# Kernel tuning notes

Hardware: AMD Instinct MI355X
Metric: run time of the kernel (lower is better)

## Reference

```python
import jax, jax.numpy as jnp
import numpy as np

N, E, NFEAT, NHID, K, TOP_N, NCLASS = 50000, 800000, 512, 128, 4, 2, 64
ALPHA = 0.2   # LeakyReLU negative slope (config.alpha)
EPS = 1e-16   # avoid 0/0 for isolated / fully-masked nodes


def _spgat_layer(h, src, dst, a, mask, concat):
    """SpGraphAttentionLayer_2: attention over given edges, no internal W.
    h: (N, F); a: (2F,); mask: optional (E,) 0/1 edge-subset mask.
    edge_e = exp(-leakyrelu(a . [h_src; h_dst]));
    out = segsum(e * h_dst) / segsum(e)  (per target node src).
    """
    F = h.shape[1]
    s1 = h @ a[:F]                     # (N,)
    s2 = h @ a[F:]                     # (N,)
    e = jnp.exp(-jax.nn.leaky_relu(s1[src] + s2[dst], ALPHA))  # (E,)
    if mask is not None:
        e = e * mask
    rowsum = jax.ops.segment_sum(e, src, num_segments=N)              # (N,)
    hp = jax.ops.segment_sum(e[:, None] * h[dst], src, num_segments=N)  # (N,F)
    hp = hp / (rowsum[:, None] + EPS)
    return jax.nn.elu(hp) if concat else hp


def setup_inputs() -> dict:
    key = jax.random.key(0)
    ks = jax.random.split(key, 7)
    x = jax.random.normal(ks[0], (N, NFEAT), jnp.float32)
    edge = jax.random.randint(ks[1], (2, E), 0, N)
    W_ks = jax.random.normal(ks[2], (K, NFEAT, NHID), jnp.float32) * 0.05
    a_k = jax.random.normal(ks[3], (K, 2 * NHID * K), jnp.float32) * 0.05
    W_o = jax.random.normal(ks[4], (NHID * K, NCLASS), jnp.float32) * 0.05
    a_att = jax.random.normal(ks[5], (K, 2 * NHID), jnp.float32) * 0.05
    a_out = jax.random.normal(ks[6], (2 * NCLASS,), jnp.float32) * 0.05
    return {"x": x, "edge": edge, "W_ks": W_ks, "a_k": a_k,
            "W_o": W_o, "a_att": a_att, "a_out": a_out}


def reference(x, edge, W_ks, a_k, W_o, a_att, a_out):
    src, dst = edge[0], edge[1]
    # K per-factor projections; dropout is a no-op in eval mode
    h_k = jnp.einsum('nf,kfh->knh', x, W_ks)              # (K, N, H)
    h = jnp.transpose(h_k, (1, 0, 2)).reshape(N, K * NHID)  # cat(h_k, dim=1)
    # Edge-level factor routing: softmax_K( a_k @ [h_src; h_dst] ).
    # Linear score => precompute per-node halves instead of (E, 2KH) gather.
    s_src = h @ a_k[:, :K * NHID].T                       # (N, K)
    s_dst = h @ a_k[:, K * NHID:].T                       # (N, K)
    edge_att = jax.nn.softmax(s_src[src] + s_dst[dst], axis=-1)  # (E, K)
    top_att, top_idx = jax.lax.top_k(edge_att, TOP_N)     # (E, TOP_N)
    # edge e belongs to factor k iff k is among its top_n factors
    masks = (top_idx[:, :, None] == jnp.arange(K)[None, None, :]).any(1)  # (E, K)
    outs = [_spgat_layer(h_k[k], src, dst, a_att[k],
                         masks[:, k].astype(h.dtype), True) for k in range(K)]
    xo = jnp.concatenate(outs, axis=1) @ W_o              # (N, NCLASS)
    xo = jax.nn.elu(_spgat_layer(xo, src, dst, a_out, None, False))
    att_loss = jnp.mean(1.0 - jnp.sum(top_att, axis=1))
    return jax.nn.log_softmax(xo, axis=1), att_loss
```

## Files before the change

kernel.cpp:

```cpp
#include <hip/hip_runtime.h>
#include <math.h>

#define NN 50000
#define NE 800000
#define NF 512
#define NH 128
#define KF 4
#define NC 64
#define LRELU_ALPHA 0.2f
#define EPSF 1e-16f

typedef unsigned short u16;
typedef __attribute__((ext_vector_type(8))) short bf16x8;
typedef __attribute__((ext_vector_type(4))) float f32x4;

#define OFF_H      0LL
#define OFF_HP     (OFF_H + (long long)NN * NF)
#define OFF_REC    (OFF_HP + (long long)NN * NF)
#define OFF_XO0    (OFF_REC + 4LL * NE)
#define OFF_SSRC   (OFF_XO0 + (long long)NN * NC)
#define OFF_SDST   (OFF_SSRC + (long long)NN * KF)
#define OFF_S1A    (OFF_SDST + (long long)NN * KF)
#define OFF_S2A    (OFF_S1A + (long long)NN * KF)
#define OFF_ROWSUM (OFF_S2A + (long long)NN * KF)
#define OFF_S1O    (OFF_ROWSUM + (long long)NN * KF)
#define OFF_S2O    (OFF_S1O + NN)
#define OFF_START  (OFF_S2O + NN)
#define OFF_CNT    (OFF_START + NN + 4)
#define OFF_CURSOR (OFF_CNT + NN)
#define OFF_ATT    (OFF_CURSOR + NN)
#define WS_FLOATS  (OFF_ATT + 2)

__device__ __forceinline__ u16 bf16_rne(float f) {
    unsigned int u = __float_as_uint(f);
    return (u16)((u + 0x7FFFu + ((u >> 16) & 1u)) >> 16);
}
__device__ __forceinline__ float bf16_f(u16 b) {
    return __uint_as_float(((unsigned int)b) << 16);
}

__device__ __forceinline__ void gload_lds16(const u16* g, u16* l) {
    __builtin_amdgcn_global_load_lds(
        (const __attribute__((address_space(1))) void*)g,
        (__attribute__((address_space(3))) void*)l, 16, 0, 0);
}

__global__ __launch_bounds__(256) void split_x(const float* __restrict__ x,
                                               u16* __restrict__ xhi,
                                               u16* __restrict__ xlo) {
    size_t i = ((size_t)blockIdx.x * 256 + threadIdx.x) * 8;
    float4 v0 = *(const float4*)(x + i);
    float4 v1 = *(const float4*)(x + i + 4);
    float v[8] = {v0.x, v0.y, v0.z, v0.w, v1.x, v1.y, v1.z, v1.w};
    unsigned int hp[4], lp[4];
#pragma unroll
    for (int j = 0; j < 4; ++j) {
        u16 h0 = bf16_rne(v[2 * j]);
        u16 h1 = bf16_rne(v[2 * j + 1]);
        u16 l0 = bf16_rne(v[2 * j] - bf16_f(h0));
        u16 l1 = bf16_rne(v[2 * j + 1] - bf16_f(h1));
        hp[j] = (unsigned int)h0 | ((unsigned int)h1 << 16);
        lp[j] = (unsigned int)l0 | ((unsigned int)l1 << 16);
    }
    *(uint4*)(xhi + i) = make_uint4(hp[0], hp[1], hp[2], hp[3]);
    *(uint4*)(xlo + i) = make_uint4(lp[0], lp[1], lp[2], lp[3]);
}

__global__ void split_w(const float* __restrict__ Wks,
                        u16* __restrict__ wthi, u16* __restrict__ wtlo) {
    int b = blockIdx.x;
    int kf = b >> 7, n = b & 127;
    for (int f = threadIdx.x; f < NF; f += 256) {
        float v = Wks[(size_t)kf * (NF * NH) + (size_t)f * NH + n];
        u16 hb = bf16_rne(v);
        u16 lb = bf16_rne(v - bf16_f(hb));
        wthi[(size_t)b * NF + f] = hb;
        wtlo[(size_t)b * NF + f] = lb;
    }
}

__global__ __launch_bounds__(256) void gemm_h_mfma(
        const u16* __restrict__ xhi, const u16* __restrict__ xlo,
        const u16* __restrict__ wthi, const u16* __restrict__ wtlo,
        float* __restrict__ h) {
    __shared__ u16 Ah[128 * 32], Al[128 * 32], Bh[128 * 32], Bl[128 * 32];
    int m0 = blockIdx.y * 128, n0 = blockIdx.x * 128;
    int tid = threadIdx.x;
    int lane = tid & 63;
    int wave = tid >> 6, wm = wave >> 1, wn = wave & 1;
    f32x4 acc[4][4];
#pragma unroll
    for (int i = 0; i < 4; ++i)
#pragma unroll
        for (int j = 0; j < 4; ++j) acc[i][j] = (f32x4)(0.f);

    u16* sbuf = (wave == 0) ? Ah : (wave == 1) ? Al : (wave == 2) ? Bh : Bl;
    const u16* gbase = (wave == 0) ? xhi : (wave == 1) ? xlo
                     : (wave == 2) ? wthi : wtlo;
    int rowbase = (wave < 2) ? m0 : n0;
    int c16s = (lane & 3) ^ ((lane >> 2) & 3) ^ (lane >> 4);
    const u16* gsrc[8];
#pragma unroll
    for (int i = 0; i < 8; ++i) {
        int rowg = rowbase + 16 * i + (lane >> 2);
        if (wave < 2 && rowg >= NN) rowg = NN - 1;
        gsrc[i] = gbase + (size_t)rowg * NF + c16s * 8;
    }

    const int arow = wm * 64 + (lane & 15);
    const int brow = wn * 64 + (lane & 15);
    const int rc16 = (lane >> 4) ^ ((lane & 3) ^ ((lane >> 2) & 3));
    const int fragoff = rc16 * 8;

    for (int k0 = 0; k0 < NF; k0 += 32) {
        __syncthreads();
#pragma unroll
        for (int i = 0; i < 8; ++i)
            gload_lds16(gsrc[i] + k0, sbuf + i * 512);
        __syncthreads();
        bf16x8 ah[4], al[4], bh[4], bl[4];
#pragma unroll
        for (int mi = 0; mi < 4; ++mi) {
            ah[mi] = *(const bf16x8*)(Ah + (arow + mi * 16) * 32 + fragoff);
            al[mi] = *(const bf16x8*)(Al + (arow + mi * 16) * 32 + fragoff);
        }
#pragma unroll
        for (int ni = 0; ni < 4; ++ni) {
            bh[ni] = *(const bf16x8*)(Bh + (brow + ni * 16) * 32 + fragoff);
            bl[ni] = *(const bf16x8*)(Bl + (brow + ni * 16) * 32 + fragoff);
        }
#pragma unroll
        for (int mi = 0; mi < 4; ++mi)
#pragma unroll
            for (int ni = 0; ni < 4; ++ni) {
                acc[mi][ni] = __builtin_amdgcn_mfma_f32_16x16x32_bf16(
                    ah[mi], bh[ni], acc[mi][ni], 0, 0, 0);
                acc[mi][ni] = __builtin_amdgcn_mfma_f32_16x16x32_bf16(
                    ah[mi], bl[ni], acc[mi][ni], 0, 0, 0);
                acc[mi][ni] = __builtin_amdgcn_mfma_f32_16x16x32_bf16(
                    al[mi], bh[ni], acc[mi][ni], 0, 0, 0);
            }
    }
#pragma unroll
    for (int mi = 0; mi < 4; ++mi) {
        int mbase = m0 + wm * 64 + mi * 16 + (lane >> 4) * 4;
#pragma unroll
        for (int ni = 0; ni < 4; ++ni) {
            int n = n0 + wn * 64 + ni * 16 + (lane & 15);
#pragma unroll
            for (int r = 0; r < 4; ++r) {
                int m = mbase + r;
                if (m < NN) h[(size_t)m * NF + n] = acc[mi][ni][r];
            }
        }
    }
}

__global__ __launch_bounds__(256) void compute_svals_h(
        const float* __restrict__ h, const float* __restrict__ a_k,
        const float* __restrict__ a_att,
        float* __restrict__ s_src, float* __restrict__ s_dst,
        float* __restrict__ s1a, float* __restrict__ s2a) {
    __shared__ float Ak[4][1024];
    __shared__ float Aa[4][256];
    for (int i = threadIdx.x; i < 4096; i += 256) Ak[i >> 10][i & 1023] = a_k[i];
    for (int i = threadIdx.x; i < 1024; i += 256) Aa[i >> 8][i & 255] = a_att[i];
    __syncthreads();
    int w = threadIdx.x >> 6, lane = threadIdx.x & 63;
    for (int n = blockIdx.x * 4 + w; n < NN; n += gridDim.x * 4) {
        const float* hr = h + (size_t)n * NF;
        float accS[4] = {0, 0, 0, 0}, accD[4] = {0, 0, 0, 0};
        float accQ1[4] = {0, 0, 0, 0}, accQ2[4] = {0, 0, 0, 0};
#pragma unroll
        for (int i = 0; i < 8; ++i) {
            int f = i * 64 + lane;
            float hv = hr[f];
#pragma unroll
            for (int k = 0; k < 4; ++k) {
                accS[k] = fmaf(hv, Ak[k][f], accS[k]);
                accD[k] = fmaf(hv, Ak[k][512 + f], accD[k]);
            }
            accQ1[i >> 1] = fmaf(hv, Aa[i >> 1][f & 127], accQ1[i >> 1]);
            accQ2[i >> 1] = fmaf(hv, Aa[i >> 1][128 + (f & 127)], accQ2[i >> 1]);
        }
#pragma unroll
        for (int off = 32; off >= 1; off >>= 1) {
#pragma unroll
            for (int k = 0; k < 4; ++k) {
                accS[k] += __shfl_xor(accS[k], off);
                accD[k] += __shfl_xor(accD[k], off);
                accQ1[k] += __shfl_xor(accQ1[k], off);
                accQ2[k] += __shfl_xor(accQ2[k], off);
            }
        }
        if (lane == 0) {
#pragma unroll
            for (int k = 0; k < 4; ++k) {
                s_src[n * 4 + k] = accS[k];
                s_dst[n * 4 + k] = accD[k];
                s1a[n * 4 + k]   = accQ1[k];
                s2a[n * 4 + k]   = accQ2[k];
            }
        }
    }
}

__global__ void csr_count(const int* __restrict__ edge, int* __restrict__ cnt) {
    int e = blockIdx.x * 256 + threadIdx.x;
    if (e < NE) atomicAdd(&cnt[edge[e]], 1);
}

__global__ __launch_bounds__(1024) void csr_scan(const int* __restrict__ cnt,
                                                 int* __restrict__ start) {
    __shared__ int part[1024];
    int t = threadIdx.x;
    const int CH = (NN + 1023) / 1024;
    int base = t * CH;
    int s = 0;
    for (int i = 0; i < CH; ++i) {
        int idx = base + i;
        if (idx < NN) s += cnt[idx];
    }
    part[t] = s;
    __syncthreads();
    for (int off = 1; off < 1024; off <<= 1) {
        int v = (t >= off) ? part[t - off] : 0;
        __syncthreads();
        part[t] += v;
        __syncthreads();
    }
    int run = (t == 0) ? 0 : part[t - 1];
    for (int i = 0; i < CH; ++i) {
        int idx = base + i;
        if (idx < NN) { start[idx] = run; run += cnt[idx]; }
    }
    if (t == 1023) start[NN] = run;
}

__global__ __launch_bounds__(256) void edge_pre1(
        const int* __restrict__ edge, const int* __restrict__ start,
        int* __restrict__ cursor,
        const float* __restrict__ s_src, const float* __restrict__ s_dst,
        const float* __restrict__ s1a, const float* __restrict__ s2a,
        int4* __restrict__ rec, double* __restrict__ att_acc) {
    __shared__ float blk[4];
    int tid = threadIdx.x;
    int e = blockIdx.x * 256 + tid;
    float t2 = 0.f;
    if (e < NE) {
        int src = edge[e];
        int dst = edge[NE + e];
        float4 ss = *(const float4*)(s_src + (size_t)src * 4);
        float4 sd = *(const float4*)(s_dst + (size_t)dst * 4);
        float l0 = ss.x + sd.x, l1 = ss.y + sd.y, l2 = ss.z + sd.z, l3 = ss.w + sd.w;
        int i1 = 0; float v1 = l0;
        if (l1 > v1) { v1 = l1; i1 = 1; }
        if (l2 > v1) { v1 = l2; i1 = 2; }
        if (l3 > v1) { v1 = l3; i1 = 3; }
        int i2 = 0; float v2 = -3.4e38f;
        if (i1 != 0)            { v2 = l0; i2 = 0; }
        if (i1 != 1 && l1 > v2) { v2 = l1; i2 = 1; }
        if (i1 != 2 && l2 > v2) { v2 = l2; i2 = 2; }
        if (i1 != 3 && l3 > v2) { v2 = l3; i2 = 3; }
        float esum = expf(l0 - v1) + expf(l1 - v1) + expf(l2 - v1) + expf(l3 - v1);
        t2 = (1.f + expf(v2 - v1)) / esum;
        float4 q1 = *(const float4*)(s1a + (size_t)src * 4);
        float4 q2 = *(const float4*)(s2a + (size_t)dst * 4);
        float q1v1 = i1 == 0 ? q1.x : i1 == 1 ? q1.y : i1 == 2 ? q1.z : q1.w;
        float q2v1 = i1 == 0 ? q2.x : i1 == 1 ? q2.y : i1 == 2 ? q2.z : q2.w;
        float q1v2 = i2 == 0 ? q1.x : i2 == 1 ? q1.y : i2 == 2 ? q1.z : q1.w;
        float q2v2 = i2 == 0 ? q2.x : i2 == 1 ? q2.y : i2 == 2 ? q2.z : q2.w;
        float sv1 = q1v1 + q2v1, sv2 = q1v2 + q2v2;
        float ee1 = expf(-(sv1 >= 0.f ? sv1 : LRELU_ALPHA * sv1));
        float ee2 = expf(-(sv2 >= 0.f ? sv2 : LRELU_ALPHA * sv2));
        int p = start[src] + atomicAdd(&cursor[src], 1);
        rec[p] = make_int4(dst, src | (i1 << 16) | (i2 << 18),
                           __float_as_int(ee1), __float_as_int(ee2));
    }
#pragma unroll
    for (int off = 32; off >= 1; off >>= 1) t2 += __shfl_xor(t2, off);
    if ((tid & 63) == 0) blk[tid >> 6] = t2;
    __syncthreads();
    if (tid == 0)
        atomicAdd(att_acc, (double)(blk[0] + blk[1] + blk[2] + blk[3]));
}

__global__ __launch_bounds__(256) void node_gather1(
        const int* __restrict__ start, const int4* __restrict__ rec,
        const float* __restrict__ h, float* __restrict__ hp,
        float* __restrict__ rowsum) {
    __shared__ float red[4][512];
    __shared__ float rsred[4][4];
    int n = blockIdx.x;
    int w = threadIdx.x >> 6, lane = threadIdx.x & 63;
    int j0 = start[n], j1 = start[n + 1];
    float a00 = 0.f, a01 = 0.f, a10 = 0.f, a11 = 0.f;
    float a20 = 0.f, a21 = 0.f, a30 = 0.f, a31 = 0.f;
    float rs0 = 0.f, rs1 = 0.f, rs2 = 0.f, rs3 = 0.f;
    for (int j = j0 + w; j < j1; j += 4) {
        int4 r = rec[j];
        int i1 = (r.y >> 16) & 3, i2 = (r.y >> 18) & 3;
        float w1 = __int_as_float(r.z), w2 = __int_as_float(r.w);
        const float* hr = h + (size_t)r.x * NF + lane;
        float v1a = hr[i1 * 128];
        float v1b = hr[i1 * 128 + 64];
        float v2a = hr[i2 * 128];
        float v2b = hr[i2 * 128 + 64];
        switch (i1) {
            case 0: a00 = fmaf(w1, v1a, a00); a01 = fmaf(w1, v1b, a01); rs0 += w1; break;
            case 1: a10 = fmaf(w1, v1a, a10); a11 = fmaf(w1, v1b, a11); rs1 += w1; break;
            case 2: a20 = fmaf(w1, v1a, a20); a21 = fmaf(w1, v1b, a21); rs2 += w1; break;
            default:a30 = fmaf(w1, v1a, a30); a31 = fmaf(w1, v1b, a31); rs3 += w1; break;
        }
        switch (i2) {
            case 0: a00 = fmaf(w2, v2a, a00); a01 = fmaf(w2, v2b, a01); rs0 += w2; break;
            case 1: a10 = fmaf(w2, v2a, a10); a11 = fmaf(w2, v2b, a11); rs1 += w2; break;
            case 2: a20 = fmaf(w2, v2a, a20); a21 = fmaf(w2, v2b, a21); rs2 += w2; break;
            default:a30 = fmaf(w2, v2a, a30); a31 = fmaf(w2, v2b, a31); rs3 += w2; break;
        }
    }
    red[w][lane]       = a00; red[w][64 + lane]  = a01;
    red[w][128 + lane] = a10; red[w][192 + lane] = a11;
    red[w][256 + lane] = a20; red[w][320 + lane] = a21;
    red[w][384 + lane] = a30; red[w][448 + lane] = a31;
    if (lane == 0) {
        rsred[w][0] = rs0; rsred[w][1] = rs1; rsred[w][2] = rs2; rsred[w][3] = rs3;
    }
    __syncthreads();
    int t = threadIdx.x;
    float s0 = (red[0][t] + red[1][t]) + (red[2][t] + red[3][t]);
    float s1 = (red[0][256 + t] + red[1][256 + t]) + (red[2][256 + t] + red[3][256 + t]);
    float* hpr = hp + (size_t)n * NF;
    hpr[t]       = s0;
    hpr[256 + t] = s1;
    if (t < 4)
        rowsum[n * 4 + t] = (rsred[0][t] + rsred[1][t]) + (rsred[2][t] + rsred[3][t]);
}

__global__ __launch_bounds__(256) void node_pass_gemm(
        const float* __restrict__ hp, const float* __restrict__ rowsum,
        const float* __restrict__ Wo, const float* __restrict__ a_out,
        float* __restrict__ xo0, float* __restrict__ s1o, float* __restrict__ s2o) {
    __shared__ float As[16][128];
    __shared__ float Bs[16][64];
    int m0 = blockIdx.x * 128;
    int tid = threadIdx.x;
    int tm = tid >> 4, tn = tid & 15;
    float acc[8][4];
#pragma unroll
    for (int i = 0; i < 8; ++i)
#pragma unroll
        for (int j = 0; j < 4; ++j) acc[i][j] = 0.f;

    int arow = tid >> 1;
    int akc  = (tid & 1) * 8;
    int am = m0 + arow; if (am >= NN) am = NN - 1;
    int brow = tid >> 4, bcol = (tid & 15) * 4;

    for (int k0 = 0; k0 < NF; k0 += 16) {
        float rs = rowsum[am * 4 + ((k0 + akc) >> 7)] + EPSF;
        float4 v0 = *(const float4*)(hp + (size_t)am * NF + k0 + akc);
        float4 v1 = *(const float4*)(hp + (size_t)am * NF + k0 + akc + 4);
        float v[8] = {v0.x, v0.y, v0.z, v0.w, v1.x, v1.y, v1.z, v1.w};
#pragma unroll
        for (int i = 0; i < 8; ++i) {
            float t = v[i] / rs;
            v[i] = t > 0.f ? t : expm1f(t);
        }
        As[akc + 0][arow] = v[0]; As[akc + 1][arow] = v[1];
        As[akc + 2][arow] = v[2]; As[akc + 3][arow] = v[3];
        As[akc + 4][arow] = v[4]; As[akc + 5][arow] = v[5];
        As[akc + 6][arow] = v[6]; As[akc + 7][arow] = v[7];
        *(float4*)&Bs[brow][bcol] =
            *(const float4*)(Wo + (size_t)(k0 + brow) * NC + bcol);
        __syncthreads();
#pragma unroll
        for (int kk = 0; kk < 16; ++kk) {
            float4 av0 = *(float4*)&As[kk][tm * 8];
            float4 av1 = *(float4*)&As[kk][tm * 8 + 4];
            float4 bv  = *(float4*)&Bs[kk][tn * 4];
            float a[8] = {av0.x, av0.y, av0.z, av0.w, av1.x, av1.y, av1.z, av1.w};
            float b[4] = {bv.x, bv.y, bv.z, bv.w};
#pragma unroll
            for (int i = 0; i < 8; ++i)
#pragma unroll
                for (int j = 0; j < 4; ++j)
                    acc[i][j] = fmaf(a[i], b[j], acc[i][j]);
        }
        __syncthreads();
    }
    float4 ao1 = *(const float4*)(a_out + tn * 4);
    float4 ao2 = *(const float4*)(a_out + 64 + tn * 4);
#pragma unroll
    for (int i = 0; i < 8; ++i) {
        int m = m0 + tm * 8 + i;
        float4 o = make_float4(acc[i][0], acc[i][1], acc[i][2], acc[i][3]);
        float p1 = o.x * ao1.x + o.y * ao1.y + o.z * ao1.z + o.w * ao1.w;
        float p2 = o.x * ao2.x + o.y * ao2.y + o.z * ao2.z + o.w * ao2.w;
#pragma unroll
        for (int off = 8; off >= 1; off >>= 1) {
            p1 += __shfl_xor(p1, off);
            p2 += __shfl_xor(p2, off);
        }
        if (m < NN) {
            *(float4*)(xo0 + (size_t)m * NC + tn * 4) = o;
            if (tn == 0) { s1o[m] = p1; s2o[m] = p2; }
        }
    }
}

__global__ __launch_bounds__(256) void node_gather2(
        const int* __restrict__ start, const int4* __restrict__ rec,
        const float* __restrict__ s1o, const float* __restrict__ s2o,
        const float* __restrict__ xo0, float* __restrict__ out) {
    __shared__ float red[4][64];
    __shared__ float rsl[4];
    int n = blockIdx.x;
    int w = threadIdx.x >> 6, lane = threadIdx.x & 63;
    int j0 = start[n], j1 = start[n + 1];
    float s1n = s1o[n];
    float acc = 0.f, rsum = 0.f;
    for (int j = j0 + w; j < j1; j += 4) {
        int d = rec[j].x;
        float sv = s1n + s2o[d];
        float e = expf(-(sv >= 0.f ? sv : LRELU_ALPHA * sv));
        acc = fmaf(e, xo0[(size_t)d * NC + lane], acc);
        rsum += e;
    }
    red[w][lane] = acc;
    if (lane == 0) rsl[w] = rsum;
    __syncthreads();
    if (w == 0) {
        float a = (red[0][lane] + red[1][lane]) + (red[2][lane] + red[3][lane]);
        float r = (rsl[0] + rsl[1]) + (rsl[2] + rsl[3]);
        float t = a / (r + EPSF);
        float v = t > 0.f ? t : expm1f(t);
        float m = v;
#pragma unroll
        for (int off = 32; off >= 1; off >>= 1) m = fmaxf(m, __shfl_xor(m, off));
        float p = expf(v - m);
#pragma unroll
        for (int off = 32; off >= 1; off >>= 1) p += __shfl_xor(p, off);
        out[(size_t)n * NC + lane] = v - m - logf(p);
    }
}

__global__ void finalize_att(const double* __restrict__ att_acc, float* __restrict__ out) {
    out[(size_t)NN * NC] = 1.f - (float)(att_acc[0] / (double)NE);
}

extern "C" void kernel_launch(void* const* d_in, const int* in_sizes, int n_in,
                              void* d_out, int out_size, void* d_ws, size_t ws_size,
                              hipStream_t stream) {
    const float* x     = (const float*)d_in[0];
    const int*   edge  = (const int*)d_in[1];
    const float* Wks   = (const float*)d_in[2];
    const float* a_k   = (const float*)d_in[3];
    const float* Wo    = (const float*)d_in[4];
    const float* a_att = (const float*)d_in[5];
    const float* a_out = (const float*)d_in[6];
    float* out = (float*)d_out;

    float* wsf = (float*)d_ws;
    float* h      = wsf + OFF_H;
    float* hp     = wsf + OFF_HP;
    int4*  rec    = (int4*)(wsf + OFF_REC);
    float* xo0    = wsf + OFF_XO0;
    float* s_src  = wsf + OFF_SSRC;
    float* s_dst  = wsf + OFF_SDST;
    float* s1a    = wsf + OFF_S1A;
    float* s2a    = wsf + OFF_S2A;
    float* rowsum = wsf + OFF_ROWSUM;
    float* s1o    = wsf + OFF_S1O;
    float* s2o    = wsf + OFF_S2O;
    int*   startp = (int*)(wsf + OFF_START);
    int*   cnt    = (int*)(wsf + OFF_CNT);
    int*   cursor = (int*)(wsf + OFF_CURSOR);
    double* att   = (double*)(wsf + OFF_ATT);

    u16* xhi  = (u16*)(wsf + OFF_HP);
    u16* xlo  = xhi + (size_t)NN * NF;
    u16* wthi = (u16*)(wsf + OFF_REC);
    u16* wtlo = wthi + (size_t)KF * NH * NF;

    size_t zero_bytes = (size_t)(WS_FLOATS - OFF_CNT) * sizeof(float);
    hipMemsetAsync((char*)d_ws + (size_t)OFF_CNT * sizeof(float), 0, zero_bytes, stream);

    split_x<<<(NN * NF / 8 + 255) / 256, 256, 0, stream>>>(x, xhi, xlo);
    split_w<<<KF * NH, 256, 0, stream>>>(Wks, wthi, wtlo);
    gemm_h_mfma<<<dim3(4, (NN + 127) / 128), 256, 0, stream>>>(xhi, xlo, wthi, wtlo, h);
    compute_svals_h<<<256, 256, 0, stream>>>(h, a_k, a_att,
                                             s_src, s_dst, s1a, s2a);
    csr_count<<<(NE + 255) / 256, 256, 0, stream>>>(edge, cnt);
    csr_scan<<<1, 1024, 0, stream>>>(cnt, startp);
    edge_pre1<<<(NE + 255) / 256, 256, 0, stream>>>(edge, startp, cursor,
                                                    s_src, s_dst, s1a, s2a, rec, att);
    node_gather1<<<NN, 256, 0, stream>>>(startp, rec, h, hp, rowsum);
    node_pass_gemm<<<(NN + 127) / 128, 256, 0, stream>>>(hp, rowsum, Wo, a_out,
                                                         xo0, s1o, s2o);
    node_gather2<<<NN, 256, 0, stream>>>(startp, rec, s1o, s2o, xo0, out);
    finalize_att<<<1, 1, 0, stream>>>(att, out);
}
```

Baseline: 723.7 us.

## Use split-bf16 MFMA for output GEMM and fuse small launches

Replaces the fp32 FMA output projection with a split-bf16 (hi/lo, three-product) MFMA GEMM. The gather now writes the normalised, ELU-activated features directly as bf16 hi/lo pairs instead of fp32 hp plus rowsum. The edge count is merged into the x-split kernel, the Wo split into split_w, and finalize_att into a new dots_out kernel. The main GEMM grid is also remapped so consecutive tiles land on the same XCD for L2 locality. This cuts launch count and the fp32 output-GEMM cost, at the price of an extra pass over xo0 for the attention dot products and small precision differences from the split-bf16 products.

```diff
diff --git a/kernel.cpp b/kernel.cpp
--- a/kernel.cpp
+++ b/kernel.cpp
@@ -22,8 +22,8 @@
 #define OFF_SDST   (OFF_SSRC + (long long)NN * KF)
 #define OFF_S1A    (OFF_SDST + (long long)NN * KF)
 #define OFF_S2A    (OFF_S1A + (long long)NN * KF)
-#define OFF_ROWSUM (OFF_S2A + (long long)NN * KF)
-#define OFF_S1O    (OFF_ROWSUM + (long long)NN * KF)
+#define OFF_WOT    (OFF_S2A + (long long)NN * KF)
+#define OFF_S1O    (OFF_WOT + (long long)NN * KF)
 #define OFF_S2O    (OFF_S1O + NN)
 #define OFF_START  (OFF_S2O + NN)
 #define OFF_CNT    (OFF_START + NN + 4)
@@ -45,37 +45,55 @@
         (__attribute__((address_space(3))) void*)l, 16, 0, 0);
 }
 
-__global__ __launch_bounds__(256) void split_x(const float* __restrict__ x,
-                                               u16* __restrict__ xhi,
-                                               u16* __restrict__ xlo) {
-    size_t i = ((size_t)blockIdx.x * 256 + threadIdx.x) * 8;
-    float4 v0 = *(const float4*)(x + i);
-    float4 v1 = *(const float4*)(x + i + 4);
-    float v[8] = {v0.x, v0.y, v0.z, v0.w, v1.x, v1.y, v1.z, v1.w};
-    unsigned int hp[4], lp[4];
-#pragma unroll
-    for (int j = 0; j < 4; ++j) {
-        u16 h0 = bf16_rne(v[2 * j]);
-        u16 h1 = bf16_rne(v[2 * j + 1]);
-        u16 l0 = bf16_rne(v[2 * j] - bf16_f(h0));
-        u16 l1 = bf16_rne(v[2 * j + 1] - bf16_f(h1));
-        hp[j] = (unsigned int)h0 | ((unsigned int)h1 << 16);
-        lp[j] = (unsigned int)l0 | ((unsigned int)l1 << 16);
-    }
-    *(uint4*)(xhi + i) = make_uint4(hp[0], hp[1], hp[2], hp[3]);
-    *(uint4*)(xlo + i) = make_uint4(lp[0], lp[1], lp[2], lp[3]);
-}
-
-__global__ void split_w(const float* __restrict__ Wks,
-                        u16* __restrict__ wthi, u16* __restrict__ wtlo) {
+#define NSPLIT 12500
+__global__ __launch_bounds__(256) void split_x_count(
+        const float* __restrict__ x, u16* __restrict__ xhi, u16* __restrict__ xlo,
+        const int* __restrict__ edge, int* __restrict__ cnt) {
+    if (blockIdx.x < NSPLIT) {
+        size_t i = ((size_t)blockIdx.x * 256 + threadIdx.x) * 8;
+        float4 v0 = *(const float4*)(x + i);
+        float4 v1 = *(const float4*)(x + i + 4);
+        float v[8] = {v0.x, v0.y, v0.z, v0.w, v1.x, v1.y, v1.z, v1.w};
+        unsigned int hp[4], lp[4];
+#pragma unroll
+        for (int j = 0; j < 4; ++j) {
+            u16 h0 = bf16_rne(v[2 * j]);
+            u16 h1 = bf16_rne(v[2 * j + 1]);
+            u16 l0 = bf16_rne(v[2 * j] - bf16_f(h0));
+            u16 l1 = bf16_rne(v[2 * j + 1] - bf16_f(h1));
+            hp[j] = (unsigned int)h0 | ((unsigned int)h1 << 16);
+            lp[j] = (unsigned int)l0 | ((unsigned int)l1 << 16);
+        }
+        *(uint4*)(xhi + i) = make_uint4(hp[0], hp[1], hp[2], hp[3]);
+        *(uint4*)(xlo + i) = make_uint4(lp[0], lp[1], lp[2], lp[3]);
+    } else {
+        int e = (blockIdx.x - NSPLIT) * 256 + threadIdx.x;
+        if (e < NE) atomicAdd(&cnt[edge[e]], 1);
+    }
+}
+
+__global__ void split_w(const float* __restrict__ Wks, const float* __restrict__ Wo,
+                        u16* __restrict__ wthi, u16* __restrict__ wtlo,
+                        u16* __restrict__ wohi, u16* __restrict__ wolo) {
     int b = blockIdx.x;
-    int kf = b >> 7, n = b & 127;
-    for (int f = threadIdx.x; f < NF; f += 256) {
-        float v = Wks[(size_t)kf * (NF * NH) + (size_t)f * NH + n];
-        u16 hb = bf16_rne(v);
-        u16 lb = bf16_rne(v - bf16_f(hb));
-        wthi[(size_t)b * NF + f] = hb;
-        wtlo[(size_t)b * NF + f] = lb;
+    if (b < 512) {
+        int kf = b >> 7, n = b & 127;
+        for (int f = threadIdx.x; f < NF; f += 256) {
+            float v = Wks[(size_t)kf * (NF * NH) + (size_t)f * NH + n];
+            u16 hb = bf16_rne(v);
+            u16 lb = bf16_rne(v - bf16_f(hb));
+            wthi[(size_t)b * NF + f] = hb;
+            wtlo[(size_t)b * NF + f] = lb;
+        }
+    } else {
+        int n = b - 512;
+        for (int f = threadIdx.x; f < NF; f += 256) {
+            float v = Wo[(size_t)f * NC + n];
+            u16 hb = bf16_rne(v);
+            u16 lb = bf16_rne(v - bf16_f(hb));
+            wohi[(size_t)n * NF + f] = hb;
+            wolo[(size_t)n * NF + f] = lb;
+        }
     }
 }
 
@@ -84,7 +102,13 @@
         const u16* __restrict__ wthi, const u16* __restrict__ wtlo,
         float* __restrict__ h) {
     __shared__ u16 Ah[128 * 32], Al[128 * 32], Bh[128 * 32], Bl[128 * 32];
-    int m0 = blockIdx.y * 128, n0 = blockIdx.x * 128;
+    const int nwg = 4 * ((NN + 127) / 128);
+    const int q = nwg / 8, r = nwg % 8;
+    int o = blockIdx.x;
+    int xcd = o & 7, pos = o >> 3;
+    int wg = (xcd < r ? xcd * (q + 1) : r * (q + 1) + (xcd - r) * q) + pos;
+    int m0 = (wg >> 2) * 128, n0 = (wg & 3) * 128;
+
     int tid = threadIdx.x;
     int lane = tid & 63;
     int wave = tid >> 6, wm = wave >> 1, wn = wave & 1;
@@ -148,9 +172,9 @@
         for (int ni = 0; ni < 4; ++ni) {
             int n = n0 + wn * 64 + ni * 16 + (lane & 15);
 #pragma unroll
-            for (int r = 0; r < 4; ++r) {
-                int m = mbase + r;
-                if (m < NN) h[(size_t)m * NF + n] = acc[mi][ni][r];
+            for (int r2 = 0; r2 < 4; ++r2) {
+                int m = mbase + r2;
+                if (m < NN) h[(size_t)m * NF + n] = acc[mi][ni][r2];
             }
         }
     }
@@ -203,11 +227,6 @@
             }
         }
     }
-}
-
-__global__ void csr_count(const int* __restrict__ edge, int* __restrict__ cnt) {
-    int e = blockIdx.x * 256 + threadIdx.x;
-    if (e < NE) atomicAdd(&cnt[edge[e]], 1);
 }
 
 __global__ __launch_bounds__(1024) void csr_scan(const int* __restrict__ cnt,
@@ -287,8 +306,8 @@
 
 __global__ __launch_bounds__(256) void node_gather1(
         const int* __restrict__ start, const int4* __restrict__ rec,
-        const float* __restrict__ h, float* __restrict__ hp,
-        float* __restrict__ rowsum) {
+        const float* __restrict__ h,
+        u16* __restrict__ ahi, u16* __restrict__ alo) {
     __shared__ float red[4][512];
     __shared__ float rsred[4][4];
     int n = blockIdx.x;
@@ -330,83 +349,113 @@
     int t = threadIdx.x;
     float s0 = (red[0][t] + red[1][t]) + (red[2][t] + red[3][t]);
     float s1 = (red[0][256 + t] + red[1][256 + t]) + (red[2][256 + t] + red[3][256 + t]);
-    float* hpr = hp + (size_t)n * NF;
-    hpr[t]       = s0;
-    hpr[256 + t] = s1;
-    if (t < 4)
-        rowsum[n * 4 + t] = (rsred[0][t] + rsred[1][t]) + (rsred[2][t] + rsred[3][t]);
-}
-
-__global__ __launch_bounds__(256) void node_pass_gemm(
-        const float* __restrict__ hp, const float* __restrict__ rowsum,
-        const float* __restrict__ Wo, const float* __restrict__ a_out,
-        float* __restrict__ xo0, float* __restrict__ s1o, float* __restrict__ s2o) {
-    __shared__ float As[16][128];
-    __shared__ float Bs[16][64];
+    int f0 = t >> 7, f1 = 2 + (t >> 7);
+    float rsa = (rsred[0][f0] + rsred[1][f0]) + (rsred[2][f0] + rsred[3][f0]) + EPSF;
+    float rsb = (rsred[0][f1] + rsred[1][f1]) + (rsred[2][f1] + rsred[3][f1]) + EPSF;
+    float e0 = s0 / rsa; e0 = e0 > 0.f ? e0 : expm1f(e0);
+    float e1 = s1 / rsb; e1 = e1 > 0.f ? e1 : expm1f(e1);
+    u16 h0 = bf16_rne(e0), l0 = bf16_rne(e0 - bf16_f(h0));
+    u16 h1 = bf16_rne(e1), l1 = bf16_rne(e1 - bf16_f(h1));
+    u16* ah = ahi + (size_t)n * NF;
+    u16* al = alo + (size_t)n * NF;
+    ah[t] = h0; ah[256 + t] = h1;
+    al[t] = l0; al[256 + t] = l1;
+}
+
+__global__ __launch_bounds__(256) void node_pass_mfma(
+        const u16* __restrict__ ahi, const u16* __restrict__ alo,
+        const u16* __restrict__ wohi, const u16* __restrict__ wolo,
+        float* __restrict__ xo0) {
+    __shared__ u16 Ah[128 * 32], Al[128 * 32], Bh[64 * 32], Bl[64 * 32];
     int m0 = blockIdx.x * 128;
     int tid = threadIdx.x;
-    int tm = tid >> 4, tn = tid & 15;
-    float acc[8][4];
-#pragma unroll
-    for (int i = 0; i < 8; ++i)
-#pragma unroll
-        for (int j = 0; j < 4; ++j) acc[i][j] = 0.f;
-
-    int arow = tid >> 1;
-    int akc  = (tid & 1) * 8;
-    int am = m0 + arow; if (am >= NN) am = NN - 1;
-    int brow = tid >> 4, bcol = (tid & 15) * 4;
-
-    for (int k0 = 0; k0 < NF; k0 += 16) {
-        float rs = rowsum[am * 4 + ((k0 + akc) >> 7)] + EPSF;
-        float4 v0 = *(const float4*)(hp + (size_t)am * NF + k0 + akc);
-        float4 v1 = *(const float4*)(hp + (size_t)am * NF + k0 + akc + 4);
-        float v[8] = {v0.x, v0.y, v0.z, v0.w, v1.x, v1.y, v1.z, v1.w};
-#pragma unroll
-        for (int i = 0; i < 8; ++i) {
-            float t = v[i] / rs;
-            v[i] = t > 0.f ? t : expm1f(t);
-        }
-        As[akc + 0][arow] = v[0]; As[akc + 1][arow] = v[1];
-        As[akc + 2][arow] = v[2]; As[akc + 3][arow] = v[3];
-        As[akc + 4][arow] = v[4]; As[akc + 5][arow] = v[5];
-        As[akc + 6][arow] = v[6]; As[akc + 7][arow] = v[7];
-        *(float4*)&Bs[brow][bcol] =
-            *(const float4*)(Wo + (size_t)(k0 + brow) * NC + bcol);
+    int lane = tid & 63;
+    int wave = tid >> 6, wm = wave >> 1, wn = wave & 1;
+    f32x4 acc[4][2];
+#pragma unroll
+    for (int i = 0; i < 4; ++i)
+#pragma unroll
+        for (int j = 0; j < 2; ++j) acc[i][j] = (f32x4)(0.f);
+
+    u16* sbuf = (wave == 0) ? Ah : (wave == 1) ? Al : (wave == 2) ? Bh : Bl;
+    const u16* gbase = (wave == 0) ? ahi : (wave == 1) ? alo
+                     : (wave == 2) ? wohi : wolo;
+    int nld = (wave < 2) ? 8 : 4;
+    int c16s = (lane & 3) ^ ((lane >> 2) & 3) ^ (lane >> 4);
+    const u16* gsrc[8];
+#pragma unroll
+    for (int i = 0; i < 8; ++i) {
+        int rowg = ((wave < 2) ? m0 : 0) + 16 * i + (lane >> 2);
+        if (wave < 2 && rowg >= NN) rowg = NN - 1;
+        gsrc[i] = gbase + (size_t)rowg * NF + c16s * 8;
+    }
+
+    const int arow = wm * 64 + (lane & 15);
+    const int brow = wn * 32 + (lane & 15);
+    const int rc16 = (lane >> 4) ^ ((lane & 3) ^ ((lane >> 2) & 3));
+    const int fragoff = rc16 * 8;
+
+    for (int k0 = 0; k0 < NF; k0 += 32) {
         __syncthreads();
-#pragma unroll
-        for (int kk = 0; kk < 16; ++kk) {
-            float4 av0 = *(float4*)&As[kk][tm * 8];
-            float4 av1 = *(float4*)&As[kk][tm * 8 + 4];
-            float4 bv  = *(float4*)&Bs[kk][tn * 4];
-            float a[8] = {av0.x, av0.y, av0.z, av0.w, av1.x, av1.y, av1.z, av1.w};
-            float b[4] = {bv.x, bv.y, bv.z, bv.w};
-#pragma unroll
-            for (int i = 0; i < 8; ++i)
-#pragma unroll
-                for (int j = 0; j < 4; ++j)
-                    acc[i][j] = fmaf(a[i], b[j], acc[i][j]);
-        }
+        for (int i = 0; i < nld; ++i)
+            gload_lds16(gsrc[i] + k0, sbuf + i * 512);
         __syncthreads();
-    }
-    float4 ao1 = *(const float4*)(a_out + tn * 4);
-    float4 ao2 = *(const float4*)(a_out + 64 + tn * 4);
-#pragma unroll
-    for (int i = 0; i < 8; ++i) {
-        int m = m0 + tm * 8 + i;
-        float4 o = make_float4(acc[i][0], acc[i][1], acc[i][2], acc[i][3]);
-        float p1 = o.x * ao1.x + o.y * ao1.y + o.z * ao1.z + o.w * ao1.w;
-        float p2 = o.x * ao2.x + o.y * ao2.y + o.z * ao2.z + o.w * ao2.w;
-#pragma unroll
-        for (int off = 8; off >= 1; off >>= 1) {
-            p1 += __shfl_xor(p1, off);
-            p2 += __shfl_xor(p2, off);
-        }
-        if (m < NN) {
-            *(float4*)(xo0 + (size_t)m * NC + tn * 4) = o;
-            if (tn == 0) { s1o[m] = p1; s2o[m] = p2; }
-        }
-    }
+        bf16x8 ah[4], al[4], bh[2], bl[2];
+#pragma unroll
+        for (int mi = 0; mi < 4; ++mi) {
+            ah[mi] = *(const bf16x8*)(Ah + (arow + mi * 16) * 32 + fragoff);
+            al[mi] = *(const bf16x8*)(Al + (arow + mi * 16) * 32 + fragoff);
+        }
+#pragma unroll
+        for (int ni = 0; ni < 2; ++ni) {
+            bh[ni] = *(const bf16x8*)(Bh + (brow + ni * 16) * 32 + fragoff);
+            bl[ni] = *(const bf16x8*)(Bl + (brow + ni * 16) * 32 + fragoff);
+        }
+#pragma unroll
+        for (int mi = 0; mi < 4; ++mi)
+#pragma unroll
+            for (int ni = 0; ni < 2; ++ni) {
+                acc[mi][ni] = __builtin_amdgcn_mfma_f32_16x16x32_bf16(
+                    ah[mi], bh[ni], acc[mi][ni], 0, 0, 0);
+                acc[mi][ni] = __builtin_amdgcn_mfma_f32_16x16x32_bf16(
+                    ah[mi], bl[ni], acc[mi][ni], 0, 0, 0);
+                acc[mi][ni] = __builtin_amdgcn_mfma_f32_16x16x32_bf16(
+                    al[mi], bh[ni], acc[mi][ni], 0, 0, 0);
+            }
+    }
+#pragma unroll
+    for (int mi = 0; mi < 4; ++mi) {
+        int mbase = m0 + wm * 64 + mi * 16 + (lane >> 4) * 4;
+#pragma unroll
+        for (int ni = 0; ni < 2; ++ni) {
+            int n = wn * 32 + ni * 16 + (lane & 15);
+#pragma unroll
+            for (int r2 = 0; r2 < 4; ++r2) {
+                int m = mbase + r2;
+                if (m < NN) xo0[(size_t)m * NC + n] = acc[mi][ni][r2];
+            }
+        }
+    }
+}
+
+__global__ __launch_bounds__(256) void dots_out(
+        const float* __restrict__ xo0, const float* __restrict__ a_out,
+        const double* __restrict__ att_acc,
+        float* __restrict__ s1o, float* __restrict__ s2o, float* __restrict__ out) {
+    if (blockIdx.x == 0 && threadIdx.x == 0)
+        out[(size_t)NN * NC] = 1.f - (float)(att_acc[0] / (double)NE);
+    int w = threadIdx.x >> 6, lane = threadIdx.x & 63;
+    int n = blockIdx.x * 4 + w;
+    if (n >= NN) return;
+    float v = xo0[(size_t)n * NC + lane];
+    float p1 = v * a_out[lane];
+    float p2 = v * a_out[64 + lane];
+#pragma unroll
+    for (int off = 32; off >= 1; off >>= 1) {
+        p1 += __shfl_xor(p1, off);
+        p2 += __shfl_xor(p2, off);
+    }
+    if (lane == 0) { s1o[n] = p1; s2o[n] = p2; }
 }
 
 __global__ __launch_bounds__(256) void node_gather2(
@@ -445,10 +494,6 @@
     }
 }
 
-__global__ void finalize_att(const double* __restrict__ att_acc, float* __restrict__ out) {
-    out[(size_t)NN * NC] = 1.f - (float)(att_acc[0] / (double)NE);
-}
-
 extern "C" void kernel_launch(void* const* d_in, const int* in_sizes, int n_in,
                               void* d_out, int out_size, void* d_ws, size_t ws_size,
                               hipStream_t stream) {
@@ -463,14 +508,12 @@
 
     float* wsf = (float*)d_ws;
     float* h      = wsf + OFF_H;
-    float* hp     = wsf + OFF_HP;
     int4*  rec    = (int4*)(wsf + OFF_REC);
     float* xo0    = wsf + OFF_XO0;
     float* s_src  = wsf + OFF_SSRC;
     float* s_dst  = wsf + OFF_SDST;
     float* s1a    = wsf + OFF_S1A;
     float* s2a    = wsf + OFF_S2A;
-    float* rowsum = wsf + OFF_ROWSUM;
     float* s1o    = wsf + OFF_S1O;
     float* s2o    = wsf + OFF_S2O;
     int*   startp = (int*)(wsf + OFF_START);
@@ -480,24 +523,25 @@
 
     u16* xhi  = (u16*)(wsf + OFF_HP);
     u16* xlo  = xhi + (size_t)NN * NF;
+    u16* ahi  = xhi;
+    u16* alo  = xlo;
     u16* wthi = (u16*)(wsf + OFF_REC);
     u16* wtlo = wthi + (size_t)KF * NH * NF;
+    u16* wohi = (u16*)(wsf + OFF_WOT);
+    u16* wolo = wohi + (size_t)NC * NF;
 
     size_t zero_bytes = (size_t)(WS_FLOATS - OFF_CNT) * sizeof(float);
     hipMemsetAsync((char*)d_ws + (size_t)OFF_CNT * sizeof(float), 0, zero_bytes, stream);
 
-    split_x<<<(NN * NF / 8 + 255) / 256, 256, 0, stream>>>(x, xhi, xlo);
-    split_w<<<KF * NH, 256, 0, stream>>>(Wks, wthi, wtlo);
-    gemm_h_mfma<<<dim3(4, (NN + 127) / 128), 256, 0, stream>>>(xhi, xlo, wthi, wtlo, h);
-    compute_svals_h<<<256, 256, 0, stream>>>(h, a_k, a_att,
-                                             s_src, s_dst, s1a, s2a);
-    csr_count<<<(NE + 255) / 256, 256, 0, stream>>>(edge, cnt);
+    split_x_count<<<NSPLIT + (NE + 255) / 256, 256, 0, stream>>>(x, xhi, xlo, edge, cnt);
+    split_w<<<512 + NC, 256, 0, stream>>>(Wks, Wo, wthi, wtlo, wohi, wolo);
     csr_scan<<<1, 1024, 0, stream>>>(cnt, startp);
+    gemm_h_mfma<<<4 * ((NN + 127) / 128), 256, 0, stream>>>(xhi, xlo, wthi, wtlo, h);
+    compute_svals_h<<<256, 256, 0, stream>>>(h, a_k, a_att, s_src, s_dst, s1a, s2a);
     edge_pre1<<<(NE + 255) / 256, 256, 0, stream>>>(edge, startp, cursor,
                                                     s_src, s_dst, s1a, s2a, rec, att);
-    node_gather1<<<NN, 256, 0, stream>>>(startp, rec, h, hp, rowsum);
-    node_pass_gemm<<<(NN + 127) / 128, 256, 0, stream>>>(hp, rowsum, Wo, a_out,
-                                                         xo0, s1o, s2o);
+    node_gather1<<<NN, 256, 0, stream>>>(startp, rec, h, ahi, alo);
+    node_pass_mfma<<<(NN + 127) / 128, 256, 0, stream>>>(ahi, alo, wohi, wolo, xo0);
+    dots_out<<<(NN + 3) / 4, 256, 0, stream>>>(xo0, a_out, att, s1o, s2o, out);
     node_gather2<<<NN, 256, 0, stream>>>(startp, rec, s1o, s2o, xo0, out);
-    finalize_att<<<1, 1, 0, stream>>>(att, out);
-}
+}
```

After: 647.9 us. -10.5%, faster.
